# Kernel tuning notes

Measured on AMD Instinct MI355X. Metric: run time of the kernel, lower is better.

## Reference

```python
import jax, jax.numpy as jnp
import numpy as np

PARA_CH = 256
FEATURE_CH = 256
PI = 3.14159  # matches the literal in the torch source


def _linear_params(key, fan_in, fan_out):
    kw, kb = jax.random.split(key)
    bound = 1.0 / np.sqrt(fan_in)
    W = jax.random.uniform(kw, (fan_in, fan_out), minval=-bound, maxval=bound, dtype=jnp.float32)
    b = jax.random.uniform(kb, (fan_out,), minval=-bound, maxval=bound, dtype=jnp.float32)
    return W, b


def setup_inputs() -> dict:
    key = jax.random.key(0)
    ks = jax.random.split(key, 6)
    feature_map = jax.random.normal(ks[0], (4, FEATURE_CH, 128, 128), dtype=jnp.float32)
    para_code = jax.random.normal(ks[1], (4, PARA_CH), dtype=jnp.float32)
    W1, b1 = _linear_params(ks[2], PARA_CH, PARA_CH)
    Ws, bs = _linear_params(ks[3], PARA_CH, FEATURE_CH)
    Wr, br = _linear_params(ks[4], PARA_CH, FEATURE_CH)
    Wt, bt = _linear_params(ks[5], PARA_CH, 2 * FEATURE_CH)
    return {"feature_map": feature_map, "para_code": para_code,
            "W1": W1, "b1": b1, "Ws": Ws, "bs": bs,
            "Wr": Wr, "br": br, "Wt": Wt, "bt": bt}


def _coord_1d(n):
    # align_corners=True-style normalized coordinates, as in make_coordinate_grid_3d
    return 2.0 * (jnp.arange(n, dtype=jnp.float32) / (n - 1)) - 1.0


def _trilinear_sample_zeros(vol, gx, gy, gz):
    """F.grid_sample 5D equivalent: mode='bilinear' (trilinear), padding_mode='zeros',
    align_corners=False. vol: [B,D,H,W] (channel dim of size 1 squeezed out);
    gx,gy,gz: [B,Do,Ho,Wo] normalized coords. Returns [B,Do,Ho,Wo]."""
    B, D, H, W = vol.shape
    ix = ((gx + 1.0) * W - 1.0) * 0.5
    iy = ((gy + 1.0) * H - 1.0) * 0.5
    iz = ((gz + 1.0) * D - 1.0) * 0.5
    x0f, y0f, z0f = jnp.floor(ix), jnp.floor(iy), jnp.floor(iz)
    wx, wy, wz = ix - x0f, iy - y0f, iz - z0f
    x0 = x0f.astype(jnp.int32); x1 = x0 + 1
    y0 = y0f.astype(jnp.int32); y1 = y0 + 1
    z0 = z0f.astype(jnp.int32); z1 = z0 + 1
    vflat = vol.reshape(B, -1)

    def gather(zi, yi, xi):
        valid = (zi >= 0) & (zi < D) & (yi >= 0) & (yi < H) & (xi >= 0) & (xi < W)
        zc = jnp.clip(zi, 0, D - 1)
        yc = jnp.clip(yi, 0, H - 1)
        xc = jnp.clip(xi, 0, W - 1)
        flat = (zc * H + yc) * W + xc  # [B,Do,Ho,Wo]
        v = jnp.take_along_axis(vflat, flat.reshape(B, -1), axis=1).reshape(flat.shape)
        return jnp.where(valid, v, 0.0)

    out = (gather(z0, y0, x0) * (1 - wz) * (1 - wy) * (1 - wx)
           + gather(z0, y0, x1) * (1 - wz) * (1 - wy) * wx
           + gather(z0, y1, x0) * (1 - wz) * wy * (1 - wx)
           + gather(z0, y1, x1) * (1 - wz) * wy * wx
           + gather(z1, y0, x0) * wz * (1 - wy) * (1 - wx)
           + gather(z1, y0, x1) * wz * (1 - wy) * wx
           + gather(z1, y1, x0) * wz * wy * (1 - wx)
           + gather(z1, y1, x1) * wz * wy * wx)
    return out


def reference(feature_map, para_code, W1, b1, Ws, bs, Wr, br, Wt, bt):
    B, C, H, W = feature_map.shape  # C == feature_ch == depth of 3D grid
    p = jax.nn.relu(para_code @ W1 + b1)                      # [B, para_ch]
    scale = jax.nn.sigmoid(p @ Ws + bs) * 2.0                 # [B, C]
    angle = jnp.tanh(p @ Wr + br) * PI                        # [B, C]
    translation = jnp.tanh(p @ Wt + bt).reshape(B, C, 2)      # [B, C, 2]
    ca, sa = jnp.cos(angle), jnp.sin(angle)
    # rotation matrix [[cos, -sin], [sin, cos]] per (batch, channel)
    rot = jnp.stack([jnp.stack([ca, -sa], -1), jnp.stack([sa, ca], -1)], -2)  # [B,C,2,2]

    x = _coord_1d(W)  # [W]
    y = _coord_1d(H)  # [H]
    z = _coord_1d(C)  # [C] (depth == channel dim)
    grid_xy = jnp.stack(jnp.broadcast_arrays(x[None, None, :], y[None, :, None]), -1)  # [1,H,W,2] -> broadcast to [C,H,W,2]
    grid_xy = jnp.broadcast_to(grid_xy, (C, H, W, 2))

    # per-pixel affine transform: rot @ [x,y] * scale + trans
    trans_grid = jnp.einsum('bcij,chwj->bchwi', rot, grid_xy)
    trans_grid = trans_grid * scale[:, :, None, None, None] + translation[:, :, None, None, :]
    gx = trans_grid[..., 0]
    gy = trans_grid[..., 1]
    gz = jnp.broadcast_to(z[None, :, None, None], (B, C, H, W))

    return _trilinear_sample_zeros(feature_map, gx, gy, gz)  # [B,C,H,W]
```

## Files before the change

kernel.cpp:

```cpp
#include <hip/hip_runtime.h>
#include <math.h>

#define BATCH 4
#define CH    256
#define HH    128
#define WW    128
#define PC    256
#define PI_F  3.14159f
#define PLANE (HH * WW)

__global__ __launch_bounds__(1024, 8)
void adaat_fused_kernel(const float* __restrict__ fm,
                        const float* __restrict__ pc,
                        const float* __restrict__ W1, const float* __restrict__ b1,
                        const float* __restrict__ Ws, const float* __restrict__ bs,
                        const float* __restrict__ Wr, const float* __restrict__ br,
                        const float* __restrict__ Wt, const float* __restrict__ bt,
                        float* __restrict__ out) {
    __shared__ float  lds[PLANE];
    __shared__ float  p_sh[PC];
    __shared__ float  sh_head[8];
    __shared__ float4 sh_par[2];

    const int t   = threadIdx.x;
    const int bc0 = blockIdx.x * 2;
    const int b   = bc0 >> 8;

    {
        const int jj = t & 255;
        const int kk = t >> 8;
        const float* pcb = pc + b * PC + kk * 64;
        const float* w   = W1 + (kk * 64) * PC + jj;
        float acc = 0.0f;
#pragma unroll 8
        for (int i = 0; i < 64; ++i)
            acc = fmaf(pcb[i], w[i * PC], acc);
        lds[t] = acc;
    }
    __syncthreads();
    if (t < 256) {
        const float s = lds[t] + lds[256 + t] + lds[512 + t] + lds[768 + t] + b1[t];
        p_sh[t] = fmaxf(s, 0.0f);
    }
    __syncthreads();

    const int wv = t >> 6;
    const int l  = t & 63;
    if (wv < 8) {
        const int q  = wv >> 2;
        const int h  = wv & 3;
        const int cq = (bc0 + q) & (CH - 1);
        const float* wp;
        int stride;
        if      (h == 0) { wp = Ws + cq;                stride = CH;     }
        else if (h == 1) { wp = Wr + cq;                stride = CH;     }
        else             { wp = Wt + 2 * cq + (h == 3); stride = 2 * CH; }
        float dot = 0.0f;
#pragma unroll
        for (int m = 0; m < 4; ++m) {
            const int k = l + 64 * m;
            dot = fmaf(p_sh[k], wp[(size_t)k * stride], dot);
        }
#pragma unroll
        for (int off = 32; off >= 1; off >>= 1)
            dot += __shfl_xor(dot, off, 64);
        if (l == 0) sh_head[wv] = dot;
    }
    __syncthreads();

    if (t < 2) {
        const int cq = (bc0 + t) & (CH - 1);
        const float ds = sh_head[4 * t + 0] + bs[cq];
        const float dr = sh_head[4 * t + 1] + br[cq];
        const float d0 = sh_head[4 * t + 2] + bt[2 * cq];
        const float d1 = sh_head[4 * t + 3] + bt[2 * cq + 1];
        const float s   = 2.0f / (1.0f + expf(-ds));
        const float ang = tanhf(dr) * PI_F;
        float sa, ca;
        sincosf(ang, &sa, &ca);
        const float A  = s * ca, B = s * sa;
        const float Tx = tanhf(d0), Ty = tanhf(d1);
        sh_par[t] = make_float4(A * (128.0f / 127.0f),
                                B * (128.0f / 127.0f),
                                64.0f * (Tx - A + B) + 63.5f,
                                64.0f * (Ty - A - B) + 63.5f);
    }

    const int   xi = l & 7;
    const int   yj = wv * 8 + (l >> 3);
    const float yf = (float)yj;
    const float* base = fm + (size_t)b * (CH * PLANE);

    for (int it = 0; it < 2; ++it) {
        const int c = (bc0 + it) & (CH - 1);

        const float iz  = (256.0f / 255.0f) * (float)c - 0.5f;
        const float z0f = floorf(iz);
        const float fz  = iz - z0f;
        const int   z0  = (int)z0f;
        const float wz0 = (z0 >= 0)     ? (1.0f - fz) : 0.0f;
        const float wz1 = (z0 + 1 < CH) ? fz          : 0.0f;
        const float* pl0 = base + (size_t)max(z0, 0)          * PLANE;
        const float* pl1 = base + (size_t)min(z0 + 1, CH - 1) * PLANE;

        __syncthreads();

#pragma unroll
        for (int j = 0; j < 2; ++j) {
            const int f0 = 4 * (t + 1024 * (2 * j));
            const int f1 = 4 * (t + 1024 * (2 * j + 1));
            const float4 a0 = *(const float4*)(pl0 + f0);
            const float4 b0 = *(const float4*)(pl1 + f0);
            const float4 a1 = *(const float4*)(pl0 + f1);
            const float4 b1v = *(const float4*)(pl1 + f1);
            float4 c0, c1;
            c0.x = fmaf(wz0, a0.x, wz1 * b0.x);
            c0.y = fmaf(wz0, a0.y, wz1 * b0.y);
            c0.z = fmaf(wz0, a0.z, wz1 * b0.z);
            c0.w = fmaf(wz0, a0.w, wz1 * b0.w);
            c1.x = fmaf(wz0, a1.x, wz1 * b1v.x);
            c1.y = fmaf(wz0, a1.y, wz1 * b1v.y);
            c1.z = fmaf(wz0, a1.z, wz1 * b1v.z);
            c1.w = fmaf(wz0, a1.w, wz1 * b1v.w);
            const int y0 = f0 >> 7, x0 = f0 & (WW - 1);
            const int y1 = f1 >> 7, x1 = f1 & (WW - 1);
            *(float4*)&lds[y0 * WW + (x0 ^ ((y0 & 3) << 3))] = c0;
            *(float4*)&lds[y1 * WW + (x1 ^ ((y1 & 3) << 3))] = c1;
        }
        __syncthreads();

        const float4 P  = sh_par[it];
        const float  cA = P.x, cB = P.y, C0 = P.z, C1 = P.w;
        float* outp = out + (size_t)(bc0 + it) * PLANE + yj * WW;

#pragma unroll 2
        for (int k = 0; k < 16; ++k) {
            const float xf  = (float)(k * 8 + xi);
            const float ixf = fmaf(cA, xf, fmaf(-cB, yf, C0));
            const float iyf = fmaf(cB, xf, fmaf(cA, yf, C1));
            const float x0f = floorf(ixf);
            const float y0f = floorf(iyf);
            const float fx  = ixf - x0f;
            const float fy  = iyf - y0f;
            const float mx0 = (x0f >= 0.0f  && x0f < 128.0f) ? (1.0f - fx) : 0.0f;
            const float mx1 = (x0f >= -1.0f && x0f < 127.0f) ? fx          : 0.0f;
            const float my0 = (y0f >= 0.0f  && y0f < 128.0f) ? (1.0f - fy) : 0.0f;
            const float my1 = (y0f >= -1.0f && y0f < 127.0f) ? fy          : 0.0f;

            const int x0i = (int)x0f, y0i = (int)y0f;
            const int xc0 = min(max(x0i,     0), WW - 1);
            const int xc1 = min(max(x0i + 1, 0), WW - 1);
            const int yc0 = min(max(y0i,     0), HH - 1);
            const int yc1 = min(max(y0i + 1, 0), HH - 1);

            const int r0 = yc0 * WW, r1 = yc1 * WW;
            const int s0 = (yc0 & 3) << 3, s1 = (yc1 & 3) << 3;
            const float v00 = lds[r0 + (xc0 ^ s0)];
            const float v01 = lds[r0 + (xc1 ^ s0)];
            const float v10 = lds[r1 + (xc0 ^ s1)];
            const float v11 = lds[r1 + (xc1 ^ s1)];

            outp[k * 8 + xi] = my0 * (mx0 * v00 + mx1 * v01)
                             + my1 * (mx0 * v10 + mx1 * v11);
        }
    }
}

extern "C" void kernel_launch(void* const* d_in, const int* in_sizes, int n_in,
                              void* d_out, int out_size, void* d_ws, size_t ws_size,
                              hipStream_t stream) {
    const float* feature_map = (const float*)d_in[0];
    const float* para_code   = (const float*)d_in[1];
    const float* W1 = (const float*)d_in[2];
    const float* b1 = (const float*)d_in[3];
    const float* Ws = (const float*)d_in[4];
    const float* bs = (const float*)d_in[5];
    const float* Wr = (const float*)d_in[6];
    const float* br = (const float*)d_in[7];
    const float* Wt = (const float*)d_in[8];
    const float* bt = (const float*)d_in[9];

    adaat_fused_kernel<<<BATCH * CH / 2, 1024, 0, stream>>>(
        feature_map, para_code, W1, b1, Ws, bs, Wr, br, Wt, bt, (float*)d_out);
}
```

Before: 161.4 us.

## Split param MLP into separate kernel and double-buffer plane staging in sampler

Moves the per-batch MLP and head computation out of the sampling kernel into a small 4-block kernel that writes per-channel affine params to workspace, so each sampling block no longer recomputes the W1 matvec. The sampler now handles 4 channels per block with two LDS plane buffers, issuing global loads for the next plane before gathering from the current one. This is meant to hide load latency and remove redundant MLP work. The cost is an extra kernel launch with a serial dependency, 128KB of LDS per block, and higher register pressure from holding a staged plane in registers.

Result: slower. 172.5 us (+6.9%).

```diff
diff --git a/kernel.cpp b/kernel.cpp
--- a/kernel.cpp
+++ b/kernel.cpp
@@ -8,162 +8,180 @@
 #define PC    256
 #define PI_F  3.14159f
 #define PLANE (HH * WW)
-
-__global__ __launch_bounds__(1024, 8)
-void adaat_fused_kernel(const float* __restrict__ fm,
-                        const float* __restrict__ pc,
-                        const float* __restrict__ W1, const float* __restrict__ b1,
-                        const float* __restrict__ Ws, const float* __restrict__ bs,
-                        const float* __restrict__ Wr, const float* __restrict__ br,
-                        const float* __restrict__ Wt, const float* __restrict__ bt,
-                        float* __restrict__ out) {
-    __shared__ float  lds[PLANE];
-    __shared__ float  p_sh[PC];
-    __shared__ float  sh_head[8];
-    __shared__ float4 sh_par[2];
-
-    const int t   = threadIdx.x;
-    const int bc0 = blockIdx.x * 2;
-    const int b   = bc0 >> 8;
+#define NP    4
+
+__global__ __launch_bounds__(1024)
+void adaat_params_kernel(const float* __restrict__ pc,
+                         const float* __restrict__ W1, const float* __restrict__ b1,
+                         const float* __restrict__ Ws, const float* __restrict__ bs,
+                         const float* __restrict__ Wr, const float* __restrict__ br,
+                         const float* __restrict__ Wt, const float* __restrict__ bt,
+                         float4* __restrict__ params) {
+    __shared__ float red[1024];
+    __shared__ float p_sh[PC];
+    __shared__ float hd[4][PC];
+    const int b = blockIdx.x;
+    const int t = threadIdx.x;
 
     {
-        const int jj = t & 255;
-        const int kk = t >> 8;
+        const int jj = t & 255, kk = t >> 8;
         const float* pcb = pc + b * PC + kk * 64;
         const float* w   = W1 + (kk * 64) * PC + jj;
         float acc = 0.0f;
 #pragma unroll 8
         for (int i = 0; i < 64; ++i)
             acc = fmaf(pcb[i], w[i * PC], acc);
-        lds[t] = acc;
+        red[t] = acc;
+    }
+    __syncthreads();
+    if (t < 256)
+        p_sh[t] = fmaxf(red[t] + red[256 + t] + red[512 + t] + red[768 + t] + b1[t], 0.0f);
+    __syncthreads();
+
+    {
+        const int c = t & 255, h = t >> 8;
+        const float* wp; int stride;
+        if      (h == 0) { wp = Ws + c;               stride = PC;     }
+        else if (h == 1) { wp = Wr + c;               stride = PC;     }
+        else             { wp = Wt + 2 * c + (h == 3); stride = 2 * PC; }
+        float dot = 0.0f;
+#pragma unroll 8
+        for (int k = 0; k < PC; ++k)
+            dot = fmaf(p_sh[k], wp[(size_t)k * stride], dot);
+        hd[h][c] = dot;
     }
     __syncthreads();
     if (t < 256) {
-        const float s = lds[t] + lds[256 + t] + lds[512 + t] + lds[768 + t] + b1[t];
-        p_sh[t] = fmaxf(s, 0.0f);
-    }
-    __syncthreads();
-
-    const int wv = t >> 6;
-    const int l  = t & 63;
-    if (wv < 8) {
-        const int q  = wv >> 2;
-        const int h  = wv & 3;
-        const int cq = (bc0 + q) & (CH - 1);
-        const float* wp;
-        int stride;
-        if      (h == 0) { wp = Ws + cq;                stride = CH;     }
-        else if (h == 1) { wp = Wr + cq;                stride = CH;     }
-        else             { wp = Wt + 2 * cq + (h == 3); stride = 2 * CH; }
-        float dot = 0.0f;
-#pragma unroll
-        for (int m = 0; m < 4; ++m) {
-            const int k = l + 64 * m;
-            dot = fmaf(p_sh[k], wp[(size_t)k * stride], dot);
-        }
-#pragma unroll
-        for (int off = 32; off >= 1; off >>= 1)
-            dot += __shfl_xor(dot, off, 64);
-        if (l == 0) sh_head[wv] = dot;
-    }
-    __syncthreads();
-
-    if (t < 2) {
-        const int cq = (bc0 + t) & (CH - 1);
-        const float ds = sh_head[4 * t + 0] + bs[cq];
-        const float dr = sh_head[4 * t + 1] + br[cq];
-        const float d0 = sh_head[4 * t + 2] + bt[2 * cq];
-        const float d1 = sh_head[4 * t + 3] + bt[2 * cq + 1];
-        const float s   = 2.0f / (1.0f + expf(-ds));
-        const float ang = tanhf(dr) * PI_F;
+        const int c = t;
+        const float s   = 2.0f / (1.0f + expf(-(hd[0][c] + bs[c])));
+        const float ang = tanhf(hd[1][c] + br[c]) * PI_F;
         float sa, ca;
         sincosf(ang, &sa, &ca);
         const float A  = s * ca, B = s * sa;
-        const float Tx = tanhf(d0), Ty = tanhf(d1);
-        sh_par[t] = make_float4(A * (128.0f / 127.0f),
-                                B * (128.0f / 127.0f),
-                                64.0f * (Tx - A + B) + 63.5f,
-                                64.0f * (Ty - A - B) + 63.5f);
-    }
-
-    const int   xi = l & 7;
-    const int   yj = wv * 8 + (l >> 3);
+        const float Tx = tanhf(hd[2][c] + bt[2 * c]);
+        const float Ty = tanhf(hd[3][c] + bt[2 * c + 1]);
+        params[b * CH + c] = make_float4(A * (128.0f / 127.0f),
+                                         B * (128.0f / 127.0f),
+                                         64.0f * (Tx - A + B) + 63.5f,
+                                         64.0f * (Ty - A - B) + 63.5f);
+    }
+}
+
+struct Stage { float4 a[4]; float4 b[4]; };
+
+__device__ __forceinline__ Stage stage_load(const float* __restrict__ pl0,
+                                            const float* __restrict__ pl1, int t) {
+    Stage s;
+#pragma unroll
+    for (int j = 0; j < 4; ++j) {
+        const int f = 4 * (t + 1024 * j);
+        s.a[j] = *(const float4*)(pl0 + f);
+        s.b[j] = *(const float4*)(pl1 + f);
+    }
+    return s;
+}
+
+__device__ __forceinline__ void stage_store(float* __restrict__ buf, const Stage& s,
+                                            float wz0, float wz1, int t) {
+#pragma unroll
+    for (int j = 0; j < 4; ++j) {
+        const int f = 4 * (t + 1024 * j);
+        const int y = f >> 7, x = f & (WW - 1);
+        float4 c;
+        c.x = fmaf(wz0, s.a[j].x, wz1 * s.b[j].x);
+        c.y = fmaf(wz0, s.a[j].y, wz1 * s.b[j].y);
+        c.z = fmaf(wz0, s.a[j].z, wz1 * s.b[j].z);
+        c.w = fmaf(wz0, s.a[j].w, wz1 * s.b[j].w);
+        *(float4*)&buf[y * WW + (x ^ ((y & 3) << 3))] = c;
+    }
+}
+
+__device__ __forceinline__ void gather_plane(const float* __restrict__ buf,
+                                             const float4 P,
+                                             float* __restrict__ outp,
+                                             const float yf, const int xi) {
+    const float cA = P.x, cB = P.y, C0 = P.z, C1 = P.w;
+#pragma unroll 2
+    for (int k = 0; k < 16; ++k) {
+        const float xf  = (float)(k * 8 + xi);
+        const float ixf = fmaf(cA, xf, fmaf(-cB, yf, C0));
+        const float iyf = fmaf(cB, xf, fmaf(cA, yf, C1));
+        const float x0f = floorf(ixf);
+        const float y0f = floorf(iyf);
+        const float fx  = ixf - x0f;
+        const float fy  = iyf - y0f;
+        const float mx0 = (x0f >= 0.0f  && x0f < 128.0f) ? (1.0f - fx) : 0.0f;
+        const float mx1 = (x0f >= -1.0f && x0f < 127.0f) ? fx          : 0.0f;
+        const float my0 = (y0f >= 0.0f  && y0f < 128.0f) ? (1.0f - fy) : 0.0f;
+        const float my1 = (y0f >= -1.0f && y0f < 127.0f) ? fy          : 0.0f;
+
+        const int x0i = (int)x0f, y0i = (int)y0f;
+        const int xc0 = min(max(x0i,     0), WW - 1);
+        const int xc1 = min(max(x0i + 1, 0), WW - 1);
+        const int yc0 = min(max(y0i,     0), HH - 1);
+        const int yc1 = min(max(y0i + 1, 0), HH - 1);
+
+        const int r0 = yc0 * WW, r1 = yc1 * WW;
+        const int s0 = (yc0 & 3) << 3, s1 = (yc1 & 3) << 3;
+        const float v00 = buf[r0 + (xc0 ^ s0)];
+        const float v01 = buf[r0 + (xc1 ^ s0)];
+        const float v10 = buf[r1 + (xc0 ^ s1)];
+        const float v11 = buf[r1 + (xc1 ^ s1)];
+
+        outp[k * 8 + xi] = my0 * (mx0 * v00 + mx1 * v01)
+                         + my1 * (mx0 * v10 + mx1 * v11);
+    }
+}
+
+__global__ __launch_bounds__(1024, 4)
+void adaat_sample_kernel(const float* __restrict__ fm,
+                         const float4* __restrict__ params,
+                         float* __restrict__ out) {
+    __shared__ float buf[2][PLANE];
+
+    const int t   = threadIdx.x;
+    const int bc0 = blockIdx.x * NP;
+    const int b   = bc0 >> 8;
+    const int wv  = t >> 6, l = t & 63;
+    const int xi  = l & 7;
+    const int yj  = wv * 8 + (l >> 3);
     const float yf = (float)yj;
+
     const float* base = fm + (size_t)b * (CH * PLANE);
 
-    for (int it = 0; it < 2; ++it) {
-        const int c = (bc0 + it) & (CH - 1);
-
+    const float* pl0[NP]; const float* pl1[NP];
+    float w0[NP], w1[NP];
+#pragma unroll
+    for (int i = 0; i < NP; ++i) {
+        const int   c   = (bc0 + i) & (CH - 1);
         const float iz  = (256.0f / 255.0f) * (float)c - 0.5f;
-        const float z0f = floorf(iz);
-        const float fz  = iz - z0f;
-        const int   z0  = (int)z0f;
-        const float wz0 = (z0 >= 0)     ? (1.0f - fz) : 0.0f;
-        const float wz1 = (z0 + 1 < CH) ? fz          : 0.0f;
-        const float* pl0 = base + (size_t)max(z0, 0)          * PLANE;
-        const float* pl1 = base + (size_t)min(z0 + 1, CH - 1) * PLANE;
-
+        const float zf  = floorf(iz);
+        const float fz  = iz - zf;
+        const int   z0  = (int)zf;
+        w0[i]  = (z0 >= 0)     ? (1.0f - fz) : 0.0f;
+        w1[i]  = (z0 + 1 < CH) ? fz          : 0.0f;
+        pl0[i] = base + (size_t)max(z0, 0)          * PLANE;
+        pl1[i] = base + (size_t)min(z0 + 1, CH - 1) * PLANE;
+    }
+    float4 Ps[NP];
+#pragma unroll
+    for (int i = 0; i < NP; ++i) Ps[i] = params[bc0 + i];
+
+    Stage s = stage_load(pl0[0], pl1[0], t);
+    stage_store(&buf[0][0], s, w0[0], w1[0], t);
+    __syncthreads();
+
+#pragma unroll
+    for (int i = 1; i < NP; ++i) {
+        s = stage_load(pl0[i], pl1[i], t);
+        gather_plane(&buf[(i - 1) & 1][0], Ps[i - 1],
+                     out + (size_t)(bc0 + i - 1) * PLANE + yj * WW, yf, xi);
+        stage_store(&buf[i & 1][0], s, w0[i], w1[i], t);
         __syncthreads();
-
-#pragma unroll
-        for (int j = 0; j < 2; ++j) {
-            const int f0 = 4 * (t + 1024 * (2 * j));
-            const int f1 = 4 * (t + 1024 * (2 * j + 1));
-            const float4 a0 = *(const float4*)(pl0 + f0);
-            const float4 b0 = *(const float4*)(pl1 + f0);
-            const float4 a1 = *(const float4*)(pl0 + f1);
-            const float4 b1v = *(const float4*)(pl1 + f1);
-            float4 c0, c1;
-            c0.x = fmaf(wz0, a0.x, wz1 * b0.x);
-            c0.y = fmaf(wz0, a0.y, wz1 * b0.y);
-            c0.z = fmaf(wz0, a0.z, wz1 * b0.z);
-            c0.w = fmaf(wz0, a0.w, wz1 * b0.w);
-            c1.x = fmaf(wz0, a1.x, wz1 * b1v.x);
-            c1.y = fmaf(wz0, a1.y, wz1 * b1v.y);
-            c1.z = fmaf(wz0, a1.z, wz1 * b1v.z);
-            c1.w = fmaf(wz0, a1.w, wz1 * b1v.w);
-            const int y0 = f0 >> 7, x0 = f0 & (WW - 1);
-            const int y1 = f1 >> 7, x1 = f1 & (WW - 1);
-            *(float4*)&lds[y0 * WW + (x0 ^ ((y0 & 3) << 3))] = c0;
-            *(float4*)&lds[y1 * WW + (x1 ^ ((y1 & 3) << 3))] = c1;
-        }
-        __syncthreads();
-
-        const float4 P  = sh_par[it];
-        const float  cA = P.x, cB = P.y, C0 = P.z, C1 = P.w;
-        float* outp = out + (size_t)(bc0 + it) * PLANE + yj * WW;
-
-#pragma unroll 2
-        for (int k = 0; k < 16; ++k) {
-            const float xf  = (float)(k * 8 + xi);
-            const float ixf = fmaf(cA, xf, fmaf(-cB, yf, C0));
-            const float iyf = fmaf(cB, xf, fmaf(cA, yf, C1));
-            const float x0f = floorf(ixf);
-            const float y0f = floorf(iyf);
-            const float fx  = ixf - x0f;
-            const float fy  = iyf - y0f;
-            const float mx0 = (x0f >= 0.0f  && x0f < 128.0f) ? (1.0f - fx) : 0.0f;
-            const float mx1 = (x0f >= -1.0f && x0f < 127.0f) ? fx          : 0.0f;
-            const float my0 = (y0f >= 0.0f  && y0f < 128.0f) ? (1.0f - fy) : 0.0f;
-            const float my1 = (y0f >= -1.0f && y0f < 127.0f) ? fy          : 0.0f;
-
-            const int x0i = (int)x0f, y0i = (int)y0f;
-            const int xc0 = min(max(x0i,     0), WW - 1);
-            const int xc1 = min(max(x0i + 1, 0), WW - 1);
-            const int yc0 = min(max(y0i,     0), HH - 1);
-            const int yc1 = min(max(y0i + 1, 0), HH - 1);
-
-            const int r0 = yc0 * WW, r1 = yc1 * WW;
-            const int s0 = (yc0 & 3) << 3, s1 = (yc1 & 3) << 3;
-            const float v00 = lds[r0 + (xc0 ^ s0)];
-            const float v01 = lds[r0 + (xc1 ^ s0)];
-            const float v10 = lds[r1 + (xc0 ^ s1)];
-            const float v11 = lds[r1 + (xc1 ^ s1)];
-
-            outp[k * 8 + xi] = my0 * (mx0 * v00 + mx1 * v01)
-                             + my1 * (mx0 * v10 + mx1 * v11);
-        }
-    }
+    }
+
+    gather_plane(&buf[(NP - 1) & 1][0], Ps[NP - 1],
+                 out + (size_t)(bc0 + NP - 1) * PLANE + yj * WW, yf, xi);
 }
 
 extern "C" void kernel_launch(void* const* d_in, const int* in_sizes, int n_in,
@@ -180,6 +198,11 @@
     const float* Wt = (const float*)d_in[8];
     const float* bt = (const float*)d_in[9];
 
-    adaat_fused_kernel<<<BATCH * CH / 2, 1024, 0, stream>>>(
-        feature_map, para_code, W1, b1, Ws, bs, Wr, br, Wt, bt, (float*)d_out);
-}
+    float4* params = (float4*)d_ws;
+
+    adaat_params_kernel<<<BATCH, 1024, 0, stream>>>(
+        para_code, W1, b1, Ws, bs, Wr, br, Wt, bt, params);
+
+    adaat_sample_kernel<<<BATCH * CH / NP, 1024, 0, stream>>>(
+        feature_map, params, (float*)d_out);
+}
```
